# Kernel optimization log

Measured on AMD Instinct MI355X. Metric: run time of the kernel, lower is better.

Reference implementation:

```python
import jax, jax.numpy as jnp
import numpy as np

B, T, C = 2, 1024, 2048
N, K = 8, 32            # channels, latents per channel
N_HEAD, N_KV, D = 16, 4, 128  # head_dim = C // n_head; n_rep = 4
N_REP = N_HEAD // N_KV
N_LAYERS = 32


def setup_inputs() -> dict:
    key = jax.random.key(0)
    ks = jax.random.split(key, 8)
    std = 0.02
    proj_std = 0.02 / np.sqrt(2 * N_LAYERS)
    return {
        "x": jax.random.normal(ks[0], (B, T, C), jnp.float32),
        "channel_states": jax.random.normal(ks[1], (B, N, K, C), jnp.float32),
        "channel_mask": jax.random.randint(ks[2], (B, T), 0, N, jnp.int32),
        "Wq": jax.random.normal(ks[3], (C, N_HEAD * D), jnp.float32) * std,
        "Wk": jax.random.normal(ks[4], (C, N_KV * D), jnp.float32) * std,
        "Wv": jax.random.normal(ks[5], (C, N_KV * D), jnp.float32) * std,
        "Wo": jax.random.normal(ks[6], (N_HEAD * D, C), jnp.float32) * proj_std,
        "gate": jax.random.normal(ks[7], (1,), jnp.float32) * 0.02,
    }


def reference(x, channel_states, channel_mask, Wq, Wk, Wv, Wo, gate):
    # x: (B,T,C); channel_states: (B,N,K,C); channel_mask: (B,T) in [0,N)
    b, t, c = x.shape
    # Q projection, grouped for GQA: (B,T,n_kv,n_rep,D)
    q = (x @ Wq).reshape(b, t, N_KV, N_REP, D)
    # Project channel latents ONCE per channel (linear, identical math to the
    # module's redundant per-token re-projection): (B,N,K,n_kv,D)
    k = jnp.einsum("bnkc,ce->bnke", channel_states, Wk).reshape(b, N, K, N_KV, D)
    v = jnp.einsum("bnkc,ce->bnke", channel_states, Wv).reshape(b, N, K, N_KV, D)
    # Per-token channel gather: (B,T,K,n_kv,D)
    batch_idx = jnp.arange(b)[:, None]
    sel_k = k[batch_idx, channel_mask]
    sel_v = v[batch_idx, channel_mask]
    # Tiny-K attention per token; GQA expressed via grouped einsum (no repeat).
    scale = 1.0 / jnp.sqrt(jnp.asarray(D, x.dtype))
    scores = jnp.einsum("btgrd,btkgd->btgrk", q, sel_k) * scale  # (B,T,g,r,K)
    attn = jax.nn.softmax(scores, axis=-1)
    y = jnp.einsum("btgrk,btkgd->btgrd", attn, sel_v).reshape(b, t, c)
    out = (y @ Wo) * jnp.tanh(gate)
    return out


if __name__ == "__main__":
    inp = setup_inputs()
    print(reference(**inp).shape)
```

## Files before the change

kernel.cpp:

```cpp
#include <hip/hip_runtime.h>
#include <hip/hip_bf16.h>

#define BB 2
#define TT 1024
#define CC 2048
#define NCH 8
#define KLAT 32
#define NKV 4
#define NREP 4
#define DD 128
#define MROWS (BB*TT)
#define CSROWS (BB*NCH*KLAT)
#define NBUCKET 16
#define TTILE 8
#define MAXTILES (MROWS/TTILE + NBUCKET)

typedef unsigned short u16;
typedef __attribute__((ext_vector_type(8))) short bf16x8;
typedef __attribute__((ext_vector_type(4))) float f32x4;
typedef __attribute__((ext_vector_type(8))) u16 u16x8;

__device__ __forceinline__ u16 f2bf(float f) {
    unsigned int u = __builtin_bit_cast(unsigned int, f);
    u = (u + 0x7FFFu + ((u >> 16) & 1u)) >> 16;
    return (u16)u;
}

__device__ __forceinline__ void glds16(const u16* g, u16* l) {
    __builtin_amdgcn_global_load_lds(
        (const __attribute__((address_space(1))) void*)g,
        (__attribute__((address_space(3))) void*)l, 16, 0, 0);
}

#define PB_SORT 0
#define PB_X    1
#define PB_CS   (PB_X + 2048)
#define PB_WQ   (PB_CS + 512)
#define PB_WK   (PB_WQ + 1024)
#define PB_WV   (PB_WK + 256)
#define PB_WO   (PB_WV + 256)
#define PB_END  (PB_WO + 1024)

__device__ __forceinline__ void cvt_body(const float* __restrict__ in, u16* __restrict__ out,
                                         int blk, int tid) {
    int i = (blk * 256 + tid) * 8;
    float4 a = *(const float4*)(in + i);
    float4 b = *(const float4*)(in + i + 4);
    u16x8 o;
    o[0]=f2bf(a.x); o[1]=f2bf(a.y); o[2]=f2bf(a.z); o[3]=f2bf(a.w);
    o[4]=f2bf(b.x); o[5]=f2bf(b.y); o[6]=f2bf(b.z); o[7]=f2bf(b.w);
    *(u16x8*)(out + i) = o;
}

__device__ __forceinline__ void tcvt_body(const float* __restrict__ in, u16* __restrict__ out,
                                          int R, int C, int bx, int by, int tid,
                                          u16 (*tile)[65]) {
    const int c0 = bx * 64, r0 = by * 64;
    const int tx = tid & 15, ty = tid >> 4;
#pragma unroll
    for (int p = 0; p < 4; ++p) {
        int r = p * 16 + ty;
        float4 v = *(const float4*)(in + (size_t)(r0 + r) * C + c0 + tx * 4);
        tile[tx*4+0][r] = f2bf(v.x);
        tile[tx*4+1][r] = f2bf(v.y);
        tile[tx*4+2][r] = f2bf(v.z);
        tile[tx*4+3][r] = f2bf(v.w);
    }
    __syncthreads();
    const int oc = tid >> 2, op = tid & 3;
    u16* dst = out + (size_t)(c0 + oc) * R + r0 + op * 16;
    u16x8 v0, v1;
#pragma unroll
    for (int j = 0; j < 8; ++j) { v0[j] = tile[oc][op*16 + j]; v1[j] = tile[oc][op*16 + 8 + j]; }
    *(u16x8*)dst = v0;
    *(u16x8*)(dst + 8) = v1;
}

__global__ void __launch_bounds__(256)
prep_kernel(const float* __restrict__ x, const float* __restrict__ cs,
            const int* __restrict__ cm,
            const float* __restrict__ Wq, const float* __restrict__ Wk,
            const float* __restrict__ Wv, const float* __restrict__ Wo,
            u16* __restrict__ xb, u16* __restrict__ csb,
            u16* __restrict__ wqt, u16* __restrict__ wkvt, u16* __restrict__ wot,
            int* __restrict__ sorted, int4* __restrict__ tiles, int* __restrict__ ntiles)
{
    __shared__ u16 tile[64][65];
    __shared__ int cnt[NBUCKET], cur[NBUCKET];
    const int bid = blockIdx.x;
    const int tid = threadIdx.x;

    if (bid == PB_SORT) {
        if (tid < NBUCKET) cnt[tid] = 0;
        __syncthreads();
        for (int i = tid; i < MROWS; i += 256) {
            int bkt = ((i >> 10) << 3) | cm[i];
            atomicAdd(&cnt[bkt], 1);
        }
        __syncthreads();
        if (tid == 0) {
            int off = 0, nt = 0;
            for (int b2 = 0; b2 < NBUCKET; ++b2) {
                cur[b2] = off;
                for (int o = 0; o < cnt[b2]; o += TTILE)
                    tiles[nt++] = make_int4(b2, off + o, min(TTILE, cnt[b2] - o), 0);
                off += cnt[b2];
            }
            *ntiles = nt;
        }
        __syncthreads();
        for (int i = tid; i < MROWS; i += 256) {
            int bkt = ((i >> 10) << 3) | cm[i];
            int pos = atomicAdd(&cur[bkt], 1);
            sorted[pos] = i;
        }
    } else if (bid < PB_CS) {
        cvt_body(x, xb, bid - PB_X, tid);
    } else if (bid < PB_WQ) {
        cvt_body(cs, csb, bid - PB_CS, tid);
    } else if (bid < PB_WK) {
        int b2 = bid - PB_WQ;
        tcvt_body(Wq, wqt, CC, CC, b2 & 31, b2 >> 5, tid, tile);
    } else if (bid < PB_WV) {
        int b2 = bid - PB_WK;
        tcvt_body(Wk, wkvt, CC, 512, b2 & 7, b2 >> 3, tid, tile);
    } else if (bid < PB_WO) {
        int b2 = bid - PB_WV;
        tcvt_body(Wv, wkvt + (size_t)512 * CC, CC, 512, b2 & 7, b2 >> 3, tid, tile);
    } else {
        int b2 = bid - PB_WO;
        tcvt_body(Wo, wot, CC, CC, b2 & 31, b2 >> 5, tid, tile);
    }
}

#define GK 2048
__device__ __forceinline__ void gemm_core(const u16* __restrict__ A, const u16* __restrict__ Bt,
                                          u16* lds, f32x4 (*acc)[4], int kiters)
{
    constexpr int BK = 32, STAGE = 8192;
    const int tid  = threadIdx.x;
    const int wave = tid >> 6;
    const int lane = tid & 63;
    const int wm = (wave & 1) * 64;
    const int wn = (wave >> 1) * 64;
    const int ml = lane & 15;
    const int quad = lane >> 4;

#pragma unroll
    for (int i = 0; i < 4; ++i)
#pragma unroll
        for (int j = 0; j < 4; ++j) acc[i][j] = (f32x4){0.f, 0.f, 0.f, 0.f};

    const u16* aptr = A  + (size_t)(tid >> 2) * GK + (tid & 3) * 8;
    const u16* bptr = Bt + (size_t)(tid >> 2) * GK + (tid & 3) * 8;
    const int aoff = wave * 512;
    const int boff = 128 * BK + wave * 512;

#pragma unroll
    for (int s = 0; s < 3; ++s) {
        u16* base = lds + s * STAGE;
        glds16(aptr + s * BK,                   base + aoff);
        glds16(aptr + (size_t)64 * GK + s * BK, base + aoff + 2048);
        glds16(bptr + s * BK,                   base + boff);
        glds16(bptr + (size_t)64 * GK + s * BK, base + boff + 2048);
    }

    for (int it = 0; it < kiters; ++it) {
        u16* cbase = lds + (it & 3) * STAGE;
        asm volatile("s_waitcnt vmcnt(8)" ::: "memory");
        asm volatile("s_barrier" ::: "memory");
        {
            const int kn = (it + 3) * BK;
            u16* nbase = lds + ((it + 3) & 3) * STAGE;
            glds16(aptr + kn,                   nbase + aoff);
            glds16(aptr + (size_t)64 * GK + kn, nbase + aoff + 2048);
            glds16(bptr + kn,                   nbase + boff);
            glds16(bptr + (size_t)64 * GK + kn, nbase + boff + 2048);
        }
        bf16x8 afr[4], bfr[4];
#pragma unroll
        for (int i = 0; i < 4; ++i)
            afr[i] = *(const bf16x8*)&cbase[(wm + i * 16 + ml) * BK + quad * 8];
#pragma unroll
        for (int j = 0; j < 4; ++j)
            bfr[j] = *(const bf16x8*)&cbase[128 * BK + (wn + j * 16 + ml) * BK + quad * 8];
#pragma unroll
        for (int i = 0; i < 4; ++i)
#pragma unroll
            for (int j = 0; j < 4; ++j)
                acc[i][j] = __builtin_amdgcn_mfma_f32_16x16x32_bf16(afr[i], bfr[j], acc[i][j], 0, 0, 0);
    }
    asm volatile("s_waitcnt vmcnt(0)" ::: "memory");
}

__global__ void __launch_bounds__(256)
gemm_qkv_kernel(const u16* __restrict__ xb, const u16* __restrict__ wqt, u16* __restrict__ qb,
                const u16* __restrict__ csb, const u16* __restrict__ wkvt,
                float* __restrict__ kvp)
{
    constexpr int STAGE = 8192;
    __shared__ u16 lds[4 * STAGE];
    const int bid = blockIdx.x;
    const int tid = threadIdx.x;
    const int wave = tid >> 6, lane = tid & 63;
    const int wm = (wave & 1) * 64, wn = (wave >> 1) * 64;
    const int ml = lane & 15, quad = lane >> 4;

    const int swz = (bid & 7) * 32 + (bid >> 3);
    const int m0 = (swz & 15) * 128, n0 = (swz >> 4) * 128;

    f32x4 acc[4][4];
    gemm_core(xb + (size_t)m0 * GK, wqt + (size_t)n0 * GK, lds, acc, 64);

#pragma unroll
    for (int i = 0; i < 4; ++i)
#pragma unroll
        for (int j = 0; j < 4; ++j)
#pragma unroll
            for (int rr = 0; rr < 4; ++rr) {
                int gr = m0 + wm + i * 16 + quad * 4 + rr;
                int gc = n0 + wn + j * 16 + ml;
                qb[(size_t)gr * 2048 + gc] = f2bf(acc[i][j][rr]);
            }

    __syncthreads();

    const int tile = bid >> 3, ks = bid & 7;
    const int m0k = (tile & 3) * 128, n0k = (tile >> 2) * 128;
    gemm_core(csb + (size_t)m0k * GK + ks * 256,
              wkvt + (size_t)n0k * GK + ks * 256, lds, acc, 8);

    float* dst = kvp + (size_t)ks * 512 * 1024;
#pragma unroll
    for (int i = 0; i < 4; ++i)
#pragma unroll
        for (int j = 0; j < 4; ++j)
#pragma unroll
            for (int rr = 0; rr < 4; ++rr) {
                int gr = m0k + wm + i * 16 + quad * 4 + rr;
                int gc = n0k + wn + j * 16 + ml;
                dst[(size_t)gr * 1024 + gc] = acc[i][j][rr];
            }
}

__global__ void __launch_bounds__(256)
kv_combine_kernel(const float* __restrict__ kvp, u16* __restrict__ kb, u16* __restrict__ vt)
{
    const int idx = (blockIdx.x * 256 + threadIdx.x) * 4;
    const int r = idx >> 10, c0 = idx & 1023;
    float4 s = *(const float4*)(kvp + idx);
#pragma unroll
    for (int ks = 1; ks < 8; ++ks) {
        float4 p = *(const float4*)(kvp + (size_t)ks * 524288 + idx);
        s.x += p.x; s.y += p.y; s.z += p.z; s.w += p.w;
    }
    float v4[4] = {s.x, s.y, s.z, s.w};
#pragma unroll
    for (int t = 0; t < 4; ++t) {
        int c = c0 + t;
        if (c < 512) {
            kb[(size_t)r * 512 + c] = f2bf(v4[t]);
        } else {
            int g = (c - 512) >> 7, d = (c - 512) & 127;
            int bn = r >> 5, lat = r & 31;
            vt[(((size_t)bn * 4 + g) << 12) + (d << 5) + lat] = f2bf(v4[t]);
        }
    }
}

__global__ void __launch_bounds__(256)
gemm_out_kernel(const u16* __restrict__ yb, const u16* __restrict__ wot,
                float* __restrict__ out, const float* __restrict__ gate)
{
    constexpr int STAGE = 8192;
    __shared__ u16 lds[4 * STAGE];
    const int tid = threadIdx.x;
    const int wave = tid >> 6, lane = tid & 63;
    const int wm = (wave & 1) * 64, wn = (wave >> 1) * 64;
    const int ml = lane & 15, quad = lane >> 4;

    const int bid = blockIdx.x;
    const int swz = (bid & 7) * 32 + (bid >> 3);
    const int m0 = (swz & 15) * 128, n0 = (swz >> 4) * 128;

    f32x4 acc[4][4];
    gemm_core(yb + (size_t)m0 * GK, wot + (size_t)n0 * GK, lds, acc, 64);

    const float scl = tanhf(gate[0]);
#pragma unroll
    for (int i = 0; i < 4; ++i)
#pragma unroll
        for (int j = 0; j < 4; ++j)
#pragma unroll
            for (int rr = 0; rr < 4; ++rr) {
                int gr = m0 + wm + i * 16 + quad * 4 + rr;
                int gc = n0 + wn + j * 16 + ml;
                out[(size_t)gr * 2048 + gc] = acc[i][j][rr] * scl;
            }
}

#define KSTR 136
#define VSTR 40
__global__ void __launch_bounds__(64)
attn_mfma_kernel(const u16* __restrict__ qb, const u16* __restrict__ kb,
                 const u16* __restrict__ vt, const int* __restrict__ sorted,
                 const int4* __restrict__ tiles, const int* __restrict__ ntiles,
                 u16* __restrict__ yb)
{
    const int tile = blockIdx.x;
    if (tile >= *ntiles) return;
    const int g = blockIdx.y;
    const int4 td = tiles[tile];
    const int bucket = td.x, start = td.y, cnt = td.z;
    const int lane = threadIdx.x;
    const int ml = lane & 15, quad = lane >> 4;

    __shared__ u16 k_lds[32 * KSTR];
    __shared__ u16 v_lds[128 * VSTR];
    __shared__ u16 p_lds[32 * VSTR];
    __shared__ int tok_s[TTILE];

    if (lane < TTILE) tok_s[lane] = (lane < cnt) ? sorted[start + lane] : -1;

    {
        const u16* ksrc = kb + (size_t)bucket * 32 * 512 + g * 128;
        const u16* vsrc = vt + ((size_t)bucket * 4 + g) * 4096;
#pragma unroll
        for (int rr = 0; rr < 8; ++rr) {
            int f = rr * 64 + lane;
            int krow = f >> 4, kc = (f & 15) * 8;
            *(u16x8*)&k_lds[krow * KSTR + kc] = *(const u16x8*)(ksrc + (size_t)krow * 512 + kc);
            int vd = f >> 2, vc = (f & 3) * 8;
            *(u16x8*)&v_lds[vd * VSTR + vc] = *(const u16x8*)(vsrc + (size_t)f * 8);
        }
    }
    __syncthreads();

    f32x4 sc[2][2];
#pragma unroll
    for (int i = 0; i < 2; ++i)
#pragma unroll
        for (int j = 0; j < 2; ++j) sc[i][j] = (f32x4){0.f, 0.f, 0.f, 0.f};
    const int tokA = tok_s[ml & 7];
    const u16* qrow = qb + (size_t)(tokA >= 0 ? tokA : 0) * 2048 + g * 512 + (ml >> 3) * 128;
#pragma unroll
    for (int s = 0; s < 4; ++s) {
        bf16x8 bfr0 = *(const bf16x8*)&k_lds[ml * KSTR + s * 32 + quad * 8];
        bf16x8 bfr1 = *(const bf16x8*)&k_lds[(16 + ml) * KSTR + s * 32 + quad * 8];
#pragma unroll
        for (int i = 0; i < 2; ++i) {
            bf16x8 afr = *(const bf16x8*)(qrow + i * 256 + s * 32 + quad * 8);
            sc[i][0] = __builtin_amdgcn_mfma_f32_16x16x32_bf16(afr, bfr0, sc[i][0], 0, 0, 0);
            sc[i][1] = __builtin_amdgcn_mfma_f32_16x16x32_bf16(afr, bfr1, sc[i][1], 0, 0, 0);
        }
    }

    const float scale = 0.088388347648318447f;
#pragma unroll
    for (int i = 0; i < 2; ++i)
#pragma unroll
        for (int reg = 0; reg < 4; ++reg) {
            float s0 = sc[i][0][reg] * scale;
            float s1 = sc[i][1][reg] * scale;
            float mx = fmaxf(s0, s1);
            mx = fmaxf(mx, __shfl_xor(mx, 1));
            mx = fmaxf(mx, __shfl_xor(mx, 2));
            mx = fmaxf(mx, __shfl_xor(mx, 4));
            mx = fmaxf(mx, __shfl_xor(mx, 8));
            float e0 = __expf(s0 - mx), e1 = __expf(s1 - mx);
            float sm = e0 + e1;
            sm += __shfl_xor(sm, 1);
            sm += __shfl_xor(sm, 2);
            sm += __shfl_xor(sm, 4);
            sm += __shfl_xor(sm, 8);
            float inv = 1.0f / sm;
            int prow = i * 16 + quad * 4 + reg;
            p_lds[prow * VSTR + ml]      = f2bf(e0 * inv);
            p_lds[prow * VSTR + 16 + ml] = f2bf(e1 * inv);
        }
    __syncthreads();

    bf16x8 pfr[2], vfr[8];
    pfr[0] = *(const bf16x8*)&p_lds[ml * VSTR + quad * 8];
    pfr[1] = *(const bf16x8*)&p_lds[(16 + ml) * VSTR + quad * 8];
#pragma unroll
    for (int j = 0; j < 8; ++j)
        vfr[j] = *(const bf16x8*)&v_lds[(j * 16 + ml) * VSTR + quad * 8];
#pragma unroll
    for (int i = 0; i < 2; ++i)
#pragma unroll
        for (int j = 0; j < 8; ++j) {
            f32x4 o = (f32x4){0.f, 0.f, 0.f, 0.f};
            o = __builtin_amdgcn_mfma_f32_16x16x32_bf16(pfr[i], vfr[j], o, 0, 0, 0);
#pragma unroll
            for (int reg = 0; reg < 4; ++reg) {
                int m = quad * 4 + reg;
                int tok = tok_s[m & 7];
                if (tok >= 0) {
                    int r = i * 2 + (m >> 3);
                    yb[(size_t)tok * 2048 + g * 512 + r * 128 + j * 16 + ml] = f2bf(o[reg]);
                }
            }
        }
}

extern "C" void kernel_launch(void* const* d_in, const int* in_sizes, int n_in,
                              void* d_out, int out_size, void* d_ws, size_t ws_size,
                              hipStream_t stream) {
    const float* x    = (const float*)d_in[0];
    const float* cs   = (const float*)d_in[1];
    const int*   cm   = (const int*)d_in[2];
    const float* Wq   = (const float*)d_in[3];
    const float* Wk   = (const float*)d_in[4];
    const float* Wv   = (const float*)d_in[5];
    const float* Wo   = (const float*)d_in[6];
    const float* gate = (const float*)d_in[7];
    float* out = (float*)d_out;

    char* w = (char*)d_ws;
    u16* xb   = (u16*)w;  w += (size_t)MROWS * CC * 2;
    u16* wqt  = (u16*)w;  w += (size_t)CC * CC * 2;
    u16* wot  = (u16*)w;  w += (size_t)CC * CC * 2;
    u16* qb   = (u16*)w;  w += (size_t)MROWS * CC * 2;
    u16* csb  = (u16*)w;  w += (size_t)CSROWS * CC * 2;
    u16* wkvt = (u16*)w;  w += (size_t)1024 * CC * 2;
    u16* kb   = (u16*)w;  w += (size_t)CSROWS * 512 * 2;
    u16* vt   = (u16*)w;  w += (size_t)64 * 128 * 32 * 2;
    int* sorted = (int*)w; w += (size_t)MROWS * 4;
    int4* tiles = (int4*)w; w += (size_t)MAXTILES * 16;
    int* ntiles = (int*)w;  w += 4096;
    float* kvp = (float*)w;
    u16* yb = (u16*)w;      w += (size_t)8 * 512 * 1024 * 4;

    prep_kernel<<<PB_END, 256, 0, stream>>>(x, cs, cm, Wq, Wk, Wv, Wo,
                                            xb, csb, wqt, wkvt, wot,
                                            sorted, tiles, ntiles);
    gemm_qkv_kernel<<<256, 256, 0, stream>>>(xb, wqt, qb, csb, wkvt, kvp);
    kv_combine_kernel<<<512, 256, 0, stream>>>(kvp, kb, vt);
    attn_mfma_kernel<<<dim3(MAXTILES, 4), 64, 0, stream>>>(qb, kb, vt, sorted, tiles, ntiles, yb);
    gemm_out_kernel<<<256, 256, 0, stream>>>(yb, wot, out, gate);
}
```

Measured before the change: 189.4 us.

## Fuse all stages into one cooperative persistent kernel with grid syncs

Replaces five separate launches (prep, QKV GEMM, KV combine, attention, out GEMM) with a single cooperative kernel of 256 blocks that separates the stages with grid.sync(). The aim is to remove launch overhead and inter-kernel gaps. It also remaps GEMM tiles by XCD for locality, and makes attention read K/V straight from global memory, with one wave per KV group, instead of staging them in LDS. The cost is that every phase is limited to 256 blocks, with grid-wide barriers between phases and lower occupancy in the attention phase.

```diff
diff --git a/kernel.cpp b/kernel.cpp
--- a/kernel.cpp
+++ b/kernel.cpp
@@ -1,5 +1,8 @@
 #include <hip/hip_runtime.h>
 #include <hip/hip_bf16.h>
+#include <hip/hip_cooperative_groups.h>
+
+namespace cg = cooperative_groups;
 
 #define BB 2
 #define TT 1024
@@ -76,63 +79,6 @@
     *(u16x8*)(dst + 8) = v1;
 }
 
-__global__ void __launch_bounds__(256)
-prep_kernel(const float* __restrict__ x, const float* __restrict__ cs,
-            const int* __restrict__ cm,
-            const float* __restrict__ Wq, const float* __restrict__ Wk,
-            const float* __restrict__ Wv, const float* __restrict__ Wo,
-            u16* __restrict__ xb, u16* __restrict__ csb,
-            u16* __restrict__ wqt, u16* __restrict__ wkvt, u16* __restrict__ wot,
-            int* __restrict__ sorted, int4* __restrict__ tiles, int* __restrict__ ntiles)
-{
-    __shared__ u16 tile[64][65];
-    __shared__ int cnt[NBUCKET], cur[NBUCKET];
-    const int bid = blockIdx.x;
-    const int tid = threadIdx.x;
-
-    if (bid == PB_SORT) {
-        if (tid < NBUCKET) cnt[tid] = 0;
-        __syncthreads();
-        for (int i = tid; i < MROWS; i += 256) {
-            int bkt = ((i >> 10) << 3) | cm[i];
-            atomicAdd(&cnt[bkt], 1);
-        }
-        __syncthreads();
-        if (tid == 0) {
-            int off = 0, nt = 0;
-            for (int b2 = 0; b2 < NBUCKET; ++b2) {
-                cur[b2] = off;
-                for (int o = 0; o < cnt[b2]; o += TTILE)
-                    tiles[nt++] = make_int4(b2, off + o, min(TTILE, cnt[b2] - o), 0);
-                off += cnt[b2];
-            }
-            *ntiles = nt;
-        }
-        __syncthreads();
-        for (int i = tid; i < MROWS; i += 256) {
-            int bkt = ((i >> 10) << 3) | cm[i];
-            int pos = atomicAdd(&cur[bkt], 1);
-            sorted[pos] = i;
-        }
-    } else if (bid < PB_CS) {
-        cvt_body(x, xb, bid - PB_X, tid);
-    } else if (bid < PB_WQ) {
-        cvt_body(cs, csb, bid - PB_CS, tid);
-    } else if (bid < PB_WK) {
-        int b2 = bid - PB_WQ;
-        tcvt_body(Wq, wqt, CC, CC, b2 & 31, b2 >> 5, tid, tile);
-    } else if (bid < PB_WV) {
-        int b2 = bid - PB_WK;
-        tcvt_body(Wk, wkvt, CC, 512, b2 & 7, b2 >> 3, tid, tile);
-    } else if (bid < PB_WO) {
-        int b2 = bid - PB_WV;
-        tcvt_body(Wv, wkvt + (size_t)512 * CC, CC, 512, b2 & 7, b2 >> 3, tid, tile);
-    } else {
-        int b2 = bid - PB_WO;
-        tcvt_body(Wo, wot, CC, CC, b2 & 31, b2 >> 5, tid, tile);
-    }
-}
-
 #define GK 2048
 __device__ __forceinline__ void gemm_core(const u16* __restrict__ A, const u16* __restrict__ Bt,
                                           u16* lds, f32x4 (*acc)[4], int kiters)
@@ -194,214 +140,247 @@
 }
 
 __global__ void __launch_bounds__(256)
-gemm_qkv_kernel(const u16* __restrict__ xb, const u16* __restrict__ wqt, u16* __restrict__ qb,
-                const u16* __restrict__ csb, const u16* __restrict__ wkvt,
-                float* __restrict__ kvp)
+main_kernel(const float* __restrict__ x, const float* __restrict__ cs,
+            const int* __restrict__ cm,
+            const float* __restrict__ Wq, const float* __restrict__ Wk,
+            const float* __restrict__ Wv, const float* __restrict__ Wo,
+            const float* __restrict__ gate, float* __restrict__ out,
+            u16* __restrict__ xb, u16* __restrict__ csb,
+            u16* __restrict__ wqt, u16* __restrict__ wkvt, u16* __restrict__ wot,
+            u16* __restrict__ qb, float* __restrict__ kvp,
+            u16* __restrict__ kb, u16* __restrict__ vt, u16* __restrict__ yb,
+            int* __restrict__ sorted, int4* __restrict__ tiles, int* __restrict__ ntiles)
 {
-    constexpr int STAGE = 8192;
-    __shared__ u16 lds[4 * STAGE];
+    __shared__ __align__(16) u16 sh[32768];
+    cg::grid_group grid = cg::this_grid();
     const int bid = blockIdx.x;
     const int tid = threadIdx.x;
     const int wave = tid >> 6, lane = tid & 63;
-    const int wm = (wave & 1) * 64, wn = (wave >> 1) * 64;
     const int ml = lane & 15, quad = lane >> 4;
 
-    const int swz = (bid & 7) * 32 + (bid >> 3);
-    const int m0 = (swz & 15) * 128, n0 = (swz >> 4) * 128;
-
-    f32x4 acc[4][4];
-    gemm_core(xb + (size_t)m0 * GK, wqt + (size_t)n0 * GK, lds, acc, 64);
-
-#pragma unroll
-    for (int i = 0; i < 4; ++i)
-#pragma unroll
-        for (int j = 0; j < 4; ++j)
-#pragma unroll
-            for (int rr = 0; rr < 4; ++rr) {
-                int gr = m0 + wm + i * 16 + quad * 4 + rr;
-                int gc = n0 + wn + j * 16 + ml;
-                qb[(size_t)gr * 2048 + gc] = f2bf(acc[i][j][rr]);
-            }
-
-    __syncthreads();
-
-    const int tile = bid >> 3, ks = bid & 7;
-    const int m0k = (tile & 3) * 128, n0k = (tile >> 2) * 128;
-    gemm_core(csb + (size_t)m0k * GK + ks * 256,
-              wkvt + (size_t)n0k * GK + ks * 256, lds, acc, 8);
-
-    float* dst = kvp + (size_t)ks * 512 * 1024;
-#pragma unroll
-    for (int i = 0; i < 4; ++i)
-#pragma unroll
-        for (int j = 0; j < 4; ++j)
-#pragma unroll
-            for (int rr = 0; rr < 4; ++rr) {
-                int gr = m0k + wm + i * 16 + quad * 4 + rr;
-                int gc = n0k + wn + j * 16 + ml;
-                dst[(size_t)gr * 1024 + gc] = acc[i][j][rr];
-            }
-}
-
-__global__ void __launch_bounds__(256)
-kv_combine_kernel(const float* __restrict__ kvp, u16* __restrict__ kb, u16* __restrict__ vt)
-{
-    const int idx = (blockIdx.x * 256 + threadIdx.x) * 4;
-    const int r = idx >> 10, c0 = idx & 1023;
-    float4 s = *(const float4*)(kvp + idx);
-#pragma unroll
-    for (int ks = 1; ks < 8; ++ks) {
-        float4 p = *(const float4*)(kvp + (size_t)ks * 524288 + idx);
-        s.x += p.x; s.y += p.y; s.z += p.z; s.w += p.w;
-    }
-    float v4[4] = {s.x, s.y, s.z, s.w};
-#pragma unroll
-    for (int t = 0; t < 4; ++t) {
-        int c = c0 + t;
-        if (c < 512) {
-            kb[(size_t)r * 512 + c] = f2bf(v4[t]);
-        } else {
-            int g = (c - 512) >> 7, d = (c - 512) & 127;
-            int bn = r >> 5, lat = r & 31;
-            vt[(((size_t)bn * 4 + g) << 12) + (d << 5) + lat] = f2bf(v4[t]);
-        }
-    }
-}
-
-__global__ void __launch_bounds__(256)
-gemm_out_kernel(const u16* __restrict__ yb, const u16* __restrict__ wot,
-                float* __restrict__ out, const float* __restrict__ gate)
-{
-    constexpr int STAGE = 8192;
-    __shared__ u16 lds[4 * STAGE];
-    const int tid = threadIdx.x;
-    const int wave = tid >> 6, lane = tid & 63;
-    const int wm = (wave & 1) * 64, wn = (wave >> 1) * 64;
-    const int ml = lane & 15, quad = lane >> 4;
-
-    const int bid = blockIdx.x;
-    const int swz = (bid & 7) * 32 + (bid >> 3);
-    const int m0 = (swz & 15) * 128, n0 = (swz >> 4) * 128;
-
-    f32x4 acc[4][4];
-    gemm_core(yb + (size_t)m0 * GK, wot + (size_t)n0 * GK, lds, acc, 64);
-
-    const float scl = tanhf(gate[0]);
-#pragma unroll
-    for (int i = 0; i < 4; ++i)
-#pragma unroll
-        for (int j = 0; j < 4; ++j)
-#pragma unroll
-            for (int rr = 0; rr < 4; ++rr) {
-                int gr = m0 + wm + i * 16 + quad * 4 + rr;
-                int gc = n0 + wn + j * 16 + ml;
-                out[(size_t)gr * 2048 + gc] = acc[i][j][rr] * scl;
-            }
-}
-
-#define KSTR 136
-#define VSTR 40
-__global__ void __launch_bounds__(64)
-attn_mfma_kernel(const u16* __restrict__ qb, const u16* __restrict__ kb,
-                 const u16* __restrict__ vt, const int* __restrict__ sorted,
-                 const int4* __restrict__ tiles, const int* __restrict__ ntiles,
-                 u16* __restrict__ yb)
-{
-    const int tile = blockIdx.x;
-    if (tile >= *ntiles) return;
-    const int g = blockIdx.y;
-    const int4 td = tiles[tile];
-    const int bucket = td.x, start = td.y, cnt = td.z;
-    const int lane = threadIdx.x;
-    const int ml = lane & 15, quad = lane >> 4;
-
-    __shared__ u16 k_lds[32 * KSTR];
-    __shared__ u16 v_lds[128 * VSTR];
-    __shared__ u16 p_lds[32 * VSTR];
-    __shared__ int tok_s[TTILE];
-
-    if (lane < TTILE) tok_s[lane] = (lane < cnt) ? sorted[start + lane] : -1;
-
     {
-        const u16* ksrc = kb + (size_t)bucket * 32 * 512 + g * 128;
-        const u16* vsrc = vt + ((size_t)bucket * 4 + g) * 4096;
-#pragma unroll
-        for (int rr = 0; rr < 8; ++rr) {
-            int f = rr * 64 + lane;
-            int krow = f >> 4, kc = (f & 15) * 8;
-            *(u16x8*)&k_lds[krow * KSTR + kc] = *(const u16x8*)(ksrc + (size_t)krow * 512 + kc);
-            int vd = f >> 2, vc = (f & 3) * 8;
-            *(u16x8*)&v_lds[vd * VSTR + vc] = *(const u16x8*)(vsrc + (size_t)f * 8);
-        }
-    }
-    __syncthreads();
-
-    f32x4 sc[2][2];
-#pragma unroll
-    for (int i = 0; i < 2; ++i)
-#pragma unroll
-        for (int j = 0; j < 2; ++j) sc[i][j] = (f32x4){0.f, 0.f, 0.f, 0.f};
-    const int tokA = tok_s[ml & 7];
-    const u16* qrow = qb + (size_t)(tokA >= 0 ? tokA : 0) * 2048 + g * 512 + (ml >> 3) * 128;
-#pragma unroll
-    for (int s = 0; s < 4; ++s) {
-        bf16x8 bfr0 = *(const bf16x8*)&k_lds[ml * KSTR + s * 32 + quad * 8];
-        bf16x8 bfr1 = *(const bf16x8*)&k_lds[(16 + ml) * KSTR + s * 32 + quad * 8];
-#pragma unroll
-        for (int i = 0; i < 2; ++i) {
-            bf16x8 afr = *(const bf16x8*)(qrow + i * 256 + s * 32 + quad * 8);
-            sc[i][0] = __builtin_amdgcn_mfma_f32_16x16x32_bf16(afr, bfr0, sc[i][0], 0, 0, 0);
-            sc[i][1] = __builtin_amdgcn_mfma_f32_16x16x32_bf16(afr, bfr1, sc[i][1], 0, 0, 0);
-        }
-    }
-
-    const float scale = 0.088388347648318447f;
-#pragma unroll
-    for (int i = 0; i < 2; ++i)
-#pragma unroll
-        for (int reg = 0; reg < 4; ++reg) {
-            float s0 = sc[i][0][reg] * scale;
-            float s1 = sc[i][1][reg] * scale;
-            float mx = fmaxf(s0, s1);
-            mx = fmaxf(mx, __shfl_xor(mx, 1));
-            mx = fmaxf(mx, __shfl_xor(mx, 2));
-            mx = fmaxf(mx, __shfl_xor(mx, 4));
-            mx = fmaxf(mx, __shfl_xor(mx, 8));
-            float e0 = __expf(s0 - mx), e1 = __expf(s1 - mx);
-            float sm = e0 + e1;
-            sm += __shfl_xor(sm, 1);
-            sm += __shfl_xor(sm, 2);
-            sm += __shfl_xor(sm, 4);
-            sm += __shfl_xor(sm, 8);
-            float inv = 1.0f / sm;
-            int prow = i * 16 + quad * 4 + reg;
-            p_lds[prow * VSTR + ml]      = f2bf(e0 * inv);
-            p_lds[prow * VSTR + 16 + ml] = f2bf(e1 * inv);
-        }
-    __syncthreads();
-
-    bf16x8 pfr[2], vfr[8];
-    pfr[0] = *(const bf16x8*)&p_lds[ml * VSTR + quad * 8];
-    pfr[1] = *(const bf16x8*)&p_lds[(16 + ml) * VSTR + quad * 8];
-#pragma unroll
-    for (int j = 0; j < 8; ++j)
-        vfr[j] = *(const bf16x8*)&v_lds[(j * 16 + ml) * VSTR + quad * 8];
-#pragma unroll
-    for (int i = 0; i < 2; ++i)
-#pragma unroll
-        for (int j = 0; j < 8; ++j) {
-            f32x4 o = (f32x4){0.f, 0.f, 0.f, 0.f};
-            o = __builtin_amdgcn_mfma_f32_16x16x32_bf16(pfr[i], vfr[j], o, 0, 0, 0);
-#pragma unroll
-            for (int reg = 0; reg < 4; ++reg) {
-                int m = quad * 4 + reg;
-                int tok = tok_s[m & 7];
-                if (tok >= 0) {
-                    int r = i * 2 + (m >> 3);
-                    yb[(size_t)tok * 2048 + g * 512 + r * 128 + j * 16 + ml] = f2bf(o[reg]);
-                }
+        u16 (*tile)[65] = (u16(*)[65])sh;
+        int* cnt = (int*)(sh + 8192);
+        int* cur = cnt + NBUCKET;
+        for (int u = bid; u < PB_END; u += 256) {
+            __syncthreads();
+            if (u == PB_SORT) {
+                if (tid < NBUCKET) cnt[tid] = 0;
+                __syncthreads();
+                for (int i = tid; i < MROWS; i += 256) {
+                    int bkt = ((i >> 10) << 3) | cm[i];
+                    atomicAdd(&cnt[bkt], 1);
+                }
+                __syncthreads();
+                if (tid == 0) {
+                    int off = 0, nt = 0;
+                    for (int b2 = 0; b2 < NBUCKET; ++b2) {
+                        cur[b2] = off;
+                        for (int o = 0; o < cnt[b2]; o += TTILE)
+                            tiles[nt++] = make_int4(b2, off + o, min(TTILE, cnt[b2] - o), 0);
+                        off += cnt[b2];
+                    }
+                    *ntiles = nt;
+                }
+                __syncthreads();
+                for (int i = tid; i < MROWS; i += 256) {
+                    int bkt = ((i >> 10) << 3) | cm[i];
+                    int pos = atomicAdd(&cur[bkt], 1);
+                    sorted[pos] = i;
+                }
+            } else if (u < PB_CS) {
+                cvt_body(x, xb, u - PB_X, tid);
+            } else if (u < PB_WQ) {
+                cvt_body(cs, csb, u - PB_CS, tid);
+            } else if (u < PB_WK) {
+                int b2 = u - PB_WQ;
+                tcvt_body(Wq, wqt, CC, CC, b2 & 31, b2 >> 5, tid, tile);
+            } else if (u < PB_WV) {
+                int b2 = u - PB_WK;
+                tcvt_body(Wk, wkvt, CC, 512, b2 & 7, b2 >> 3, tid, tile);
+            } else if (u < PB_WO) {
+                int b2 = u - PB_WV;
+                tcvt_body(Wv, wkvt + (size_t)512 * CC, CC, 512, b2 & 7, b2 >> 3, tid, tile);
+            } else {
+                int b2 = u - PB_WO;
+                tcvt_body(Wo, wot, CC, CC, b2 & 31, b2 >> 5, tid, tile);
             }
         }
+    }
+    grid.sync();
+
+    {
+        const int xcd = bid & 7, l = bid >> 3;
+        const int wm = (wave & 1) * 64, wn = (wave >> 1) * 64;
+        const int m0 = ((xcd & 3) * 4 + (l & 3)) * 128;
+        const int n0 = ((xcd >> 2) * 8 + (l >> 2)) * 128;
+        f32x4 acc[4][4];
+        gemm_core(xb + (size_t)m0 * GK, wqt + (size_t)n0 * GK, sh, acc, 64);
+#pragma unroll
+        for (int i = 0; i < 4; ++i)
+#pragma unroll
+            for (int j = 0; j < 4; ++j)
+#pragma unroll
+                for (int rr = 0; rr < 4; ++rr) {
+                    int gr = m0 + wm + i * 16 + quad * 4 + rr;
+                    int gc = n0 + wn + j * 16 + ml;
+                    qb[(size_t)gr * 2048 + gc] = f2bf(acc[i][j][rr]);
+                }
+        __syncthreads();
+
+        const int m0k = (l & 3) * 128, n0k = xcd * 128, ks = l >> 2;
+        gemm_core(csb + (size_t)m0k * GK + ks * 256,
+                  wkvt + (size_t)n0k * GK + ks * 256, sh, acc, 8);
+        float* dst = kvp + (size_t)ks * 512 * 1024;
+#pragma unroll
+        for (int i = 0; i < 4; ++i)
+#pragma unroll
+            for (int j = 0; j < 4; ++j)
+#pragma unroll
+                for (int rr = 0; rr < 4; ++rr) {
+                    int gr = m0k + wm + i * 16 + quad * 4 + rr;
+                    int gc = n0k + wn + j * 16 + ml;
+                    dst[(size_t)gr * 1024 + gc] = acc[i][j][rr];
+                }
+    }
+    grid.sync();
+
+    {
+        int idx = (bid * 256 + tid) * 8;
+        int r = idx >> 10, c0 = idx & 1023;
+        float4 sa = *(const float4*)(kvp + idx);
+        float4 sb = *(const float4*)(kvp + idx + 4);
+#pragma unroll
+        for (int ks = 1; ks < 8; ++ks) {
+            const float* p = kvp + (size_t)ks * 524288 + idx;
+            float4 pa = *(const float4*)p;
+            float4 pb = *(const float4*)(p + 4);
+            sa.x += pa.x; sa.y += pa.y; sa.z += pa.z; sa.w += pa.w;
+            sb.x += pb.x; sb.y += pb.y; sb.z += pb.z; sb.w += pb.w;
+        }
+        float v8[8] = {sa.x, sa.y, sa.z, sa.w, sb.x, sb.y, sb.z, sb.w};
+        if (c0 < 512) {
+#pragma unroll
+            for (int t = 0; t < 8; ++t)
+                kb[(size_t)r * 512 + c0 + t] = f2bf(v8[t]);
+        } else {
+            int bn = r >> 5, lat = r & 31;
+#pragma unroll
+            for (int t = 0; t < 8; ++t) {
+                int c = c0 + t;
+                int g = (c - 512) >> 7, d = (c - 512) & 127;
+                vt[(((size_t)bn * 4 + g) << 12) + (d << 5) + lat] = f2bf(v8[t]);
+            }
+        }
+    }
+    grid.sync();
+
+    {
+        u16* pw = sh + wave * 1296;
+        int* tokw = (int*)(pw + 1280);
+        const int nt = *ntiles;
+        const int g = wave;
+#pragma unroll 1
+        for (int pass = 0; pass < 2; ++pass) {
+            const int tile = pass * 256 + bid;
+            if (tile >= MAXTILES || tile >= nt) continue;
+            const int4 td = tiles[tile];
+            const int bucket = td.x, start = td.y, cnt2 = td.z;
+            if (lane < TTILE) tokw[lane] = (lane < cnt2) ? sorted[start + lane] : -1;
+            asm volatile("s_waitcnt lgkmcnt(0)" ::: "memory");
+            __builtin_amdgcn_sched_barrier(0);
+
+            const u16* ksrc = kb + (size_t)bucket * 32 * 512 + g * 128;
+            const u16* vsrc = vt + ((size_t)bucket * 4 + g) * 4096;
+
+            f32x4 sc[2][2];
+#pragma unroll
+            for (int i = 0; i < 2; ++i)
+#pragma unroll
+                for (int j = 0; j < 2; ++j) sc[i][j] = (f32x4){0.f, 0.f, 0.f, 0.f};
+            const int tokA = tokw[ml & 7];
+            const u16* qrow = qb + (size_t)(tokA >= 0 ? tokA : 0) * 2048 + g * 512 + (ml >> 3) * 128;
+#pragma unroll
+            for (int s = 0; s < 4; ++s) {
+                bf16x8 bfr0 = *(const bf16x8*)(ksrc + (size_t)ml * 512 + s * 32 + quad * 8);
+                bf16x8 bfr1 = *(const bf16x8*)(ksrc + (size_t)(16 + ml) * 512 + s * 32 + quad * 8);
+#pragma unroll
+                for (int i = 0; i < 2; ++i) {
+                    bf16x8 afr = *(const bf16x8*)(qrow + i * 256 + s * 32 + quad * 8);
+                    sc[i][0] = __builtin_amdgcn_mfma_f32_16x16x32_bf16(afr, bfr0, sc[i][0], 0, 0, 0);
+                    sc[i][1] = __builtin_amdgcn_mfma_f32_16x16x32_bf16(afr, bfr1, sc[i][1], 0, 0, 0);
+                }
+            }
+
+            const float scale = 0.088388347648318447f;
+#pragma unroll
+            for (int i = 0; i < 2; ++i)
+#pragma unroll
+                for (int reg = 0; reg < 4; ++reg) {
+                    float s0 = sc[i][0][reg] * scale;
+                    float s1 = sc[i][1][reg] * scale;
+                    float mx = fmaxf(s0, s1);
+                    mx = fmaxf(mx, __shfl_xor(mx, 1));
+                    mx = fmaxf(mx, __shfl_xor(mx, 2));
+                    mx = fmaxf(mx, __shfl_xor(mx, 4));
+                    mx = fmaxf(mx, __shfl_xor(mx, 8));
+                    float e0 = __expf(s0 - mx), e1 = __expf(s1 - mx);
+                    float sm = e0 + e1;
+                    sm += __shfl_xor(sm, 1);
+                    sm += __shfl_xor(sm, 2);
+                    sm += __shfl_xor(sm, 4);
+                    sm += __shfl_xor(sm, 8);
+                    float inv = 1.0f / sm;
+                    int prow = i * 16 + quad * 4 + reg;
+                    pw[prow * 40 + ml]      = f2bf(e0 * inv);
+                    pw[prow * 40 + 16 + ml] = f2bf(e1 * inv);
+                }
+            asm volatile("s_waitcnt lgkmcnt(0)" ::: "memory");
+            __builtin_amdgcn_sched_barrier(0);
+
+            bf16x8 pfr[2];
+            pfr[0] = *(const bf16x8*)&pw[ml * 40 + quad * 8];
+            pfr[1] = *(const bf16x8*)&pw[(16 + ml) * 40 + quad * 8];
+#pragma unroll
+            for (int i = 0; i < 2; ++i)
+#pragma unroll
+                for (int j = 0; j < 8; ++j) {
+                    bf16x8 vfr = *(const bf16x8*)(vsrc + (size_t)(j * 16 + ml) * 32 + quad * 8);
+                    f32x4 o = (f32x4){0.f, 0.f, 0.f, 0.f};
+                    o = __builtin_amdgcn_mfma_f32_16x16x32_bf16(pfr[i], vfr, o, 0, 0, 0);
+#pragma unroll
+                    for (int reg = 0; reg < 4; ++reg) {
+                        int m = quad * 4 + reg;
+                        int tok = tokw[m & 7];
+                        if (tok >= 0) {
+                            int r = i * 2 + (m >> 3);
+                            yb[(size_t)tok * 2048 + g * 512 + r * 128 + j * 16 + ml] = f2bf(o[reg]);
+                        }
+                    }
+                }
+        }
+    }
+    grid.sync();
+
+    {
+        const int xcd = bid & 7, l = bid >> 3;
+        const int wm = (wave & 1) * 64, wn = (wave >> 1) * 64;
+        const int m0 = ((xcd & 3) * 4 + (l & 3)) * 128;
+        const int n0 = ((xcd >> 2) * 8 + (l >> 2)) * 128;
+        f32x4 acc[4][4];
+        gemm_core(yb + (size_t)m0 * GK, wot + (size_t)n0 * GK, sh, acc, 64);
+        const float scl = tanhf(gate[0]);
+#pragma unroll
+        for (int i = 0; i < 4; ++i)
+#pragma unroll
+            for (int j = 0; j < 4; ++j)
+#pragma unroll
+                for (int rr = 0; rr < 4; ++rr) {
+                    int gr = m0 + wm + i * 16 + quad * 4 + rr;
+                    int gc = n0 + wn + j * 16 + ml;
+                    out[(size_t)gr * 2048 + gc] = acc[i][j][rr] * scl;
+                }
+    }
 }
 
 extern "C" void kernel_launch(void* const* d_in, const int* in_sizes, int n_in,
@@ -432,11 +411,13 @@
     float* kvp = (float*)w;
     u16* yb = (u16*)w;      w += (size_t)8 * 512 * 1024 * 4;
 
-    prep_kernel<<<PB_END, 256, 0, stream>>>(x, cs, cm, Wq, Wk, Wv, Wo,
-                                            xb, csb, wqt, wkvt, wot,
-                                            sorted, tiles, ntiles);
-    gemm_qkv_kernel<<<256, 256, 0, stream>>>(xb, wqt, qb, csb, wkvt, kvp);
-    kv_combine_kernel<<<512, 256, 0, stream>>>(kvp, kb, vt);
-    attn_mfma_kernel<<<dim3(MAXTILES, 4), 64, 0, stream>>>(qb, kb, vt, sorted, tiles, ntiles, yb);
-    gemm_out_kernel<<<256, 256, 0, stream>>>(yb, wot, out, gate);
-}
+    void* kargs[] = {
+        (void*)&x, (void*)&cs, (void*)&cm, (void*)&Wq, (void*)&Wk, (void*)&Wv,
+        (void*)&Wo, (void*)&gate, (void*)&out,
+        (void*)&xb, (void*)&csb, (void*)&wqt, (void*)&wkvt, (void*)&wot,
+        (void*)&qb, (void*)&kvp, (void*)&kb, (void*)&vt, (void*)&yb,
+        (void*)&sorted, (void*)&tiles, (void*)&ntiles
+    };
+    hipLaunchCooperativeKernel((const void*)main_kernel, dim3(256), dim3(256),
+                               kargs, 0, stream);
+}
```

New measurement: 358.6 us. 1.89x slower.
